# Kernel tuning notes

Measured on AMD Instinct MI355X. Metric: run time of the kernel, lower is better.

Reference implementation:

```python
import jax, jax.numpy as jnp
import numpy as np

EPS = 1e-5
GRID = 24          # GRID_SIZE
IMG = 96           # IMAGE_SIZE[0]
SCALE = IMG / GRID # 4.0
X0, X1 = -112.0, 224.0
Y0, Y1 = 0.0, 224.0
CIN = 48
CMID = 24
NKP = 4
B = 1024


def _conv(x, w):
    # x: [B,C,H,W], w: [O,I,kh,kw]
    return jax.lax.conv_general_dilated(x, w, (1, 1), 'SAME',
                                        dimension_numbers=('NCHW', 'OIHW', 'NCHW'))


def _head(x, w1, b1, g, be, m, v, w2, b2, sig):
    y = _conv(x, w1) + b1[None, :, None, None]
    inv = jax.lax.rsqrt(v + EPS)
    y = (y - m[None, :, None, None]) * (g * inv)[None, :, None, None] + be[None, :, None, None]
    y = jax.nn.relu(y)
    y = _conv(y, w2) + b2[None, :, None, None]
    return jax.nn.sigmoid(y) if sig else y


def _head_params(key, cout):
    ks = jax.random.split(key, 4)
    w1 = jax.random.normal(ks[0], (CMID, CIN, 3, 3), jnp.float32) * 0.05
    b1 = jnp.zeros((CMID,), jnp.float32)
    g = jnp.ones((CMID,), jnp.float32)
    be = jnp.zeros((CMID,), jnp.float32)
    m = jax.random.normal(ks[1], (CMID,), jnp.float32) * 0.1
    v = jax.random.uniform(ks[2], (CMID,), jnp.float32, 0.5, 1.5)
    w2 = jax.random.normal(ks[3], (cout, CMID, 1, 1), jnp.float32) * 0.05
    b2 = jnp.zeros((cout,), jnp.float32)
    return w1, b1, g, be, m, v, w2, b2


def setup_inputs() -> dict:
    key = jax.random.key(0)
    k0, kc, kk, kr, ko = jax.random.split(key, 5)
    d = {'features': jax.random.normal(k0, (B, CIN * GRID * GRID), jnp.float32)}
    for pref, kk_, cout in (('c', kc, 1), ('k', kk, NKP), ('r', kr, 2 * NKP), ('o', ko, 2 * NKP)):
        w1, b1, g, be, m, v, w2, b2 = _head_params(kk_, cout)
        d[pref + 'w1'], d[pref + 'b1'] = w1, b1
        d[pref + 'g'], d[pref + 'be'] = g, be
        d[pref + 'm'], d[pref + 'v'] = m, v
        d[pref + 'w2'], d[pref + 'b2'] = w2, b2
    return d


def reference(features,
              cw1, cb1, cg, cbe, cm, cv, cw2, cb2,
              kw1, kb1, kg, kbe, km, kv, kw2, kb2,
              rw1, rb1, rg, rbe, rm, rv, rw2, rb2,
              ow1, ob1, og, obe, om, ov, ow2, ob2):
    Bn = features.shape[0]
    x = features.reshape(Bn, CIN, GRID, GRID)
    center = _head(x, cw1, cb1, cg, cbe, cm, cv, cw2, cb2, True)    # [B,1,H,W]
    kp = _head(x, kw1, kb1, kg, kbe, km, kv, kw2, kb2, True)        # [B,N,H,W]
    reg = _head(x, rw1, rb1, rg, rbe, rm, rv, rw2, rb2, False)      # [B,2N,H,W]
    off = _head(x, ow1, ob1, og, obe, om, ov, ow2, ob2, False)      # [B,2N,H,W]

    H = W = GRID
    hm = kp.reshape(Bn, NKP, H * W)
    idx = jnp.argmax(hm, axis=2)                                   # [B,N]
    my = (idx // W).astype(jnp.float32)
    mx = (idx % W).astype(jnp.float32)
    # offset channels: (n*2) -> x, (n*2+1) -> y
    off_r = off.reshape(Bn, NKP, 2, H * W)
    g = jnp.take_along_axis(off_r, idx[:, :, None, None], axis=3)[..., 0]  # [B,N,2]
    ox, oy = g[..., 0], g[..., 1]
    fx = (mx + ox) * SCALE + X0
    fy = (my + oy) * SCALE + Y0
    pix = jnp.stack([fx, fy], axis=-1).reshape(Bn, 2 * NKP)        # [B,8]
    norm = jnp.stack([(fx - X0) / (X1 - X0), (fy - Y0) / (Y1 - Y0)], axis=-1).reshape(Bn, 2 * NKP)
    return (center, kp, reg, off, norm, pix)
```

## Files before the change

### kernel.cpp

```cpp
#include <hip/hip_runtime.h>
#include <stdint.h>

#define HW    576
#define CIN   48
#define NB    1024

#define O_CENTER 0L
#define O_KP     589824L
#define O_REG    2949120L
#define O_OFF    7667712L
#define O_NORM   12386304L
#define O_PIX    12394496L

#define WS_A1    0
#define WS_W2A   82944
#define WS_B1A   89088
#define WS_B2A   89472
#define WS_WKPT  89600
#define WS_B1KP  131072
#define WS_W2KP  131168
#define WS_B2KP  131552
#define WS_WOFFT 131584
#define WS_B1OFF 173056
#define WS_W2OFF 173152
#define WS_B2OFF 174688

typedef short bf16x8 __attribute__((ext_vector_type(8)));
typedef float f32x16 __attribute__((ext_vector_type(16)));

union U4B  { uint4 q; bf16x8 v; };
union U16Q { uint16_t u[8]; uint4 q; };
union U4Q  { uint16_t u[4]; uint2 q; };

__device__ __forceinline__ bf16x8 as_bf(uint4 q){ U4B u; u.q = q; return u.v; }
__device__ __forceinline__ uint16_t f2b(float f){
  union { float f; uint32_t i; } x; x.f = f;
  uint32_t r = x.i + 0x7FFFu + ((x.i >> 16) & 1u);
  return (uint16_t)(r >> 16);
}

struct P32 {
  const float* w1[4]; const float* b1[4]; const float* g[4]; const float* be[4];
  const float* m[4];  const float* v[4];  const float* w2[4]; const float* b2[4];
};

__device__ __forceinline__ void oc_decode(int oc, int& h, int& ch){
  if (oc == 0){ h = 0; ch = 0; }
  else if (oc < 5){ h = 1; ch = oc - 1; }
  else if (oc < 13){ h = 2; ch = oc - 5; }
  else { h = 3; ch = oc - 13; }
}

#define PREP_BLOCKS 48
__global__ void prep_kernel(P32 P, char* __restrict__ wsb){
  const int tid = threadIdx.x, bid = blockIdx.x;
  const int g0 = bid*256 + tid;
  const int STR = PREP_BLOCKS*256;
  __shared__ float sc[96], bfold[96];
  if (tid < 96){
    int h = tid / 24, o = tid % 24;
    float s = P.g[h][o] / sqrtf(P.v[h][o] + 1e-5f);
    sc[tid] = s;
    bfold[tid] = (P.b1[h][o] - P.m[h][o]) * s + P.be[h][o];
  }
  __syncthreads();
  uint16_t* A1 = (uint16_t*)(wsb + WS_A1);
  for (int t = g0; t < 41472; t += STR){
    int j = t & 7, slot = t >> 3;
    int row = slot % 96, sk = slot / 96;
    int g = sk & 1, k3 = (sk >> 1) % 3, sh = (sk >> 1) / 3;
    int ci = k3*16 + g*8 + j;
    int h = row / 24, o = row % 24;
    A1[t] = f2b(P.w1[h][(o*CIN + ci)*9 + sh] * sc[row]);
  }
  uint16_t* W2A = (uint16_t*)(wsb + WS_W2A);
  for (int t = g0; t < 3072; t += STR){
    int j = t & 7, slot = t >> 3;
    int oc = slot & 31, kg = slot >> 5;
    int k = kg*8 + j;
    float val = 0.f;
    if (oc < 21){
      int h, ch; oc_decode(oc, h, ch);
      int hk = k / 24, o = k % 24;
      if (hk == h) val = P.w2[h][ch*24 + o];
    }
    W2A[t] = f2b(val);
  }
  float* WKPT = (float*)(wsb + WS_WKPT);
  for (int t = g0; t < 10368; t += STR){
    int o = t % 24, k = (t/24) % 9, ci = t / 216;
    WKPT[t] = P.w1[1][(o*CIN + ci)*9 + k] * sc[24 + o];
  }
  float* WOFFT = (float*)(wsb + WS_WOFFT);
  for (int t = g0; t < 10368; t += STR){
    int o = t / 432;
    WOFFT[t] = P.w1[3][t] * sc[72 + o];
  }
  if (bid == 0){
    float* B1A = (float*)(wsb + WS_B1A);
    if (tid < 96) B1A[tid] = bfold[tid];
    float* B2A = (float*)(wsb + WS_B2A);
    if (tid < 32){
      float v = 0.f;
      if (tid < 21){ int h, ch; oc_decode(tid, h, ch); v = P.b2[h][ch]; }
      B2A[tid] = v;
    }
    if (tid < 24) ((float*)(wsb + WS_B1KP))[tid] = bfold[24 + tid];
    if (tid < 96) ((float*)(wsb + WS_W2KP))[tid] = P.w2[1][tid];
    if (tid < 4)  ((float*)(wsb + WS_B2KP))[tid] = P.b2[1][tid];
    if (tid < 24) ((float*)(wsb + WS_B1OFF))[tid] = bfold[72 + tid];
    for (int t = tid; t < 384; t += 256) ((float*)(wsb + WS_W2OFF))[t] = P.w2[3][t];
    if (tid < 16) ((float*)(wsb + WS_B2OFF))[tid] = P.b2[3][tid];
  }
}

__global__ __launch_bounds__(576) void conv_main(
    const float* __restrict__ feat, const char* __restrict__ wsb,
    float* __restrict__ out)
{
  __shared__ __align__(16) char smem[60000];
  const int b = blockIdx.x, tid = threadIdx.x;
  const int wave = tid >> 6, lane = tid & 63;
  const int q = lane >> 5, l31 = lane & 31;

  if (tid < 294){
    int cib = tid / 49, r = tid % 49;
    int slot = cib*625 + ((r < 25) ? r : (r - 24)*25);
    *(uint4*)(smem + slot*16) = make_uint4(0,0,0,0);
  }
  {
    const float* fb = feat + (size_t)b * (CIN*HW);
    int p = tid, py = p / 24, px = p % 24;
    int sbase = (py+1)*25 + (px+1);
    for (int cib = 0; cib < 6; ++cib){
      U16Q t8;
      #pragma unroll
      for (int j = 0; j < 8; ++j) t8.u[j] = f2b(fb[(cib*8 + j)*HW + p]);
      *(uint4*)(smem + (cib*625 + sbase)*16) = t8.q;
    }
  }
  __syncthreads();

  f32x16 acc[3][2] = {};
  const int p0 = wave*64 + l31, p1 = p0 + 32;
  const int py0 = p0/24, px0 = p0%24, py1 = p1/24, px1 = p1%24;
  const uint4* A1 = (const uint4*)(wsb + WS_A1);
  const uint4 zz = make_uint4(0,0,0,0);

  for (int sh = 0; sh < 9; ++sh){
    const int ky = sh / 3, kx = sh % 3;
    const int yb0 = py0 + ky, xb0 = px0 + kx;
    const int yb1 = py1 + ky, xb1 = px1 + kx;
    const bool v0 = (yb0 < 25) && (xb0 < 25);
    const bool v1 = (yb1 < 25) && (xb1 < 25);
    const int so0 = yb0*25 + xb0, so1 = yb1*25 + xb1;
    #pragma unroll
    for (int k3 = 0; k3 < 3; ++k3){
      const int cib = k3*2 + q;
      uint4 r0 = *(const uint4*)(smem + (cib*625 + (v0 ? so0 : 0))*16);
      uint4 r1 = *(const uint4*)(smem + (cib*625 + (v1 ? so1 : 0))*16);
      r0 = v0 ? r0 : zz;
      r1 = v1 ? r1 : zz;
      const bf16x8 bf0 = as_bf(r0), bf1 = as_bf(r1);
      const int abase = ((sh*3 + k3)*2 + q)*96 + l31;
      #pragma unroll
      for (int mt = 0; mt < 3; ++mt){
        const bf16x8 af = as_bf(A1[abase + mt*32]);
        acc[mt][0] = __builtin_amdgcn_mfma_f32_32x32x16_bf16(af, bf0, acc[mt][0], 0, 0, 0);
        acc[mt][1] = __builtin_amdgcn_mfma_f32_32x32x16_bf16(af, bf1, acc[mt][1], 0, 0, 0);
      }
    }
  }
  __syncthreads();

  const float* B1A = (const float*)(wsb + WS_B1A);
  const float* B2A = (const float*)(wsb + WS_B2A);
  const uint4* W2A = (const uint4*)(wsb + WS_W2A);
  char* ybuf = smem + wave*6144;

  #pragma unroll
  for (int st2 = 0; st2 < 2; ++st2){
    const int p = st2 ? p1 : p0;
    #pragma unroll
    for (int mt = 0; mt < 3; ++mt){
      #pragma unroll
      for (int rg = 0; rg < 4; ++rg){
        const int chanbase = mt*32 + rg*8 + q*4;
        const float* bp = B1A + chanbase;
        U4Q t4;
        #pragma unroll
        for (int r0 = 0; r0 < 4; ++r0){
          float y = acc[mt][st2][rg*4 + r0] + bp[r0];
          t4.u[r0] = f2b(fmaxf(y, 0.f));
        }
        *(uint2*)(ybuf + ((mt*4 + rg)*32 + l31)*16 + q*8) = t4.q;
      }
    }
    f32x16 c2 = {};
    #pragma unroll
    for (int k6 = 0; k6 < 6; ++k6){
      const bf16x8 yf = as_bf(*(const uint4*)(ybuf + ((k6*2 + q)*32 + l31)*16));
      const bf16x8 wf = as_bf(W2A[(k6*2 + q)*32 + l31]);
      c2 = __builtin_amdgcn_mfma_f32_32x32x16_bf16(wf, yf, c2, 0, 0, 0);
    }
    #pragma unroll
    for (int r = 0; r < 16; ++r){
      const int oc = (r & 3) + 8*(r >> 2) + 4*q;
      if (oc < 21){
        float v = c2[r] + B2A[oc];
        long base; int sig;
        if (oc == 0){ base = O_CENTER + (long)b*HW; sig = 1; }
        else if (oc < 5){ base = O_KP + ((long)b*4 + (oc-1))*HW; sig = 1; }
        else if (oc < 13){ base = O_REG + ((long)b*8 + (oc-5))*HW; sig = 0; }
        else { base = O_OFF + ((long)b*8 + (oc-13))*HW; sig = 0; }
        out[base + p] = sig ? (1.f / (1.f + __expf(-v))) : v;
      }
    }
  }
}

__global__ __launch_bounds__(576) void kp_select(
    const float* __restrict__ feat, const char* __restrict__ wsb,
    float* __restrict__ out)
{
  __shared__ __align__(16) float simg[8*26*24];
  __shared__ float wk_lds[8*9*24];
  __shared__ float ykp [96*24];
  __shared__ __align__(16) float opatch[4][432];
  __shared__ float ymidL[4*24];
  __shared__ int   jobL[4*HW];
  __shared__ int   KtotL;
  __shared__ unsigned long long bestL[4];

  const int b = blockIdx.x, tid = threadIdx.x;
  if (tid == 0) KtotL = 0;
  if (tid < 4) bestL[tid] = 0ULL;
  __syncthreads();

  if (tid < 256){
    const int n = tid >> 6, ln = tid & 63;
    const float* sp = out + O_KP + ((long)b*4 + n)*HW;
    float s[9];
    #pragma unroll
    for (int j = 0; j < 9; ++j) s[j] = sp[j*64 + ln];
    float mx = s[0];
    #pragma unroll
    for (int j = 1; j < 9; ++j) mx = fmaxf(mx, s[j]);
    #pragma unroll
    for (int off = 32; off >= 1; off >>= 1)
      mx = fmaxf(mx, __shfl_xor(mx, off, 64));
    const float sm = fminf(mx, 0.999999f);
    const float thr = sm / (sm + (1.f - sm) * 1.1331485f);
    #pragma unroll
    for (int j = 0; j < 9; ++j){
      if (s[j] >= thr){
        const int slot = atomicAdd(&KtotL, 1);
        jobL[slot] = (n << 16) | (j*64 + ln);
      }
    }
  }
  __syncthreads();
  const int Ktot = KtotL;

  const int s24 = tid / 24, omid = tid - s24*24;
  const int dst = (s24 + 1)*24 + omid;
  const float* fb = feat + (size_t)b * (CIN*HW);
  const float* WKPT = (const float*)(wsb + WS_WKPT);
  const float b1k = ((const float*)(wsb + WS_B1KP))[omid];

  for (int g0 = 0; g0 < Ktot; g0 += 96){
    const int Kg = min(96, Ktot - g0);

    int pyc[4], pxc[4];
    #pragma unroll
    for (int c = 0; c < 4; ++c){
      int p = 0;
      if (c*24 + s24 < Kg) p = jobL[g0 + c*24 + s24] & 0xFFFF;
      pyc[c] = p / 24; pxc[c] = p - (p/24)*24;
    }

    float acck[4] = {0.f,0.f,0.f,0.f};

    for (int pass = 0; pass < 6; ++pass){
      __syncthreads();
      if (tid < 384){
        int c = tid / 48, r = tid - c*48;
        int row = (r < 24) ? 0 : 25;
        int col = (r < 24) ? r : r - 24;
        simg[c*624 + row*24 + col] = 0.f;
      }
      #pragma unroll
      for (int c = 0; c < 8; ++c)
        simg[c*624 + dst] = fb[(pass*8 + c)*HW + tid];
      #pragma unroll
      for (int j = 0; j < 3; ++j)
        wk_lds[tid + j*576] = WKPT[pass*1728 + tid + j*576];
      __syncthreads();

      for (int c8 = 0; c8 < 8; ++c8){
        float pch[4][9];
        #pragma unroll
        for (int c = 0; c < 4; ++c) if (c*24 < Kg){
          const int a = c8*624 + pyc[c]*24 + pxc[c];
          const bool wl = (pxc[c] > 0), wr = (pxc[c] < 23);
          #pragma unroll
          for (int dr = 0; dr < 3; ++dr){
            const int aa = a + dr*24;
            pch[c][dr*3+0] = wl ? simg[aa-1] : 0.f;
            pch[c][dr*3+1] = simg[aa];
            pch[c][dr*3+2] = wr ? simg[aa+1] : 0.f;
          }
        }
        const float* wkb = wk_lds + c8*216 + omid;
        #pragma unroll
        for (int k = 0; k < 9; ++k){
          const float wk = wkb[k*24];
          #pragma unroll
          for (int c = 0; c < 4; ++c) if (c*24 < Kg)
            acck[c] = fmaf(pch[c][k], wk, acck[c]);
        }
      }
    }

    #pragma unroll
    for (int c = 0; c < 4; ++c) if (c*24 < Kg){
      const int sl = c*24 + s24;
      ykp[sl*24 + omid] = fmaxf(acck[c] + b1k, 0.f);
    }
    __syncthreads();

    if (tid < Kg){
      const int cand = g0 + tid;
      const int job = jobL[cand];
      const int n = job >> 16, p = job & 0xFFFF;
      const float* W2KP = (const float*)(wsb + WS_W2KP);
      float v = ((const float*)(wsb + WS_B2KP))[n];
      #pragma unroll
      for (int o = 0; o < 24; ++o)
        v = fmaf(ykp[tid*24 + o], W2KP[n*24 + o], v);
      union { float f; uint32_t u; } cv; cv.f = v;
      const uint32_t key = cv.u ^ (uint32_t)(((int32_t)cv.u >> 31) | (int32_t)0x80000000);
      const unsigned long long pk =
          ((unsigned long long)key << 32) | (unsigned)(1023 - p);
      atomicMax(&bestL[n], pk);
    }
    __syncthreads();
  }

  #pragma unroll
  for (int j = 0; j < 3; ++j){
    const int e = tid*3 + j;
    const int w = e / 432, idx = e - w*432;
    const int ci = idx / 9, k = idx - ci*9;
    const int p = 1023 - (int)(bestL[w] & 0xFFFFFFFFu);
    const int py = p / 24, px = p % 24;
    const int yy = py + k/3 - 1, xx = px + (k - (k/3)*3) - 1;
    float v = 0.f;
    if (yy >= 0 && yy < 24 && xx >= 0 && xx < 24)
      v = fb[ci*HW + yy*24 + xx];
    opatch[w][idx] = v;
  }
  __syncthreads();

  if (tid < 96){
    const int n = tid / 24, mid = tid - n*24;
    const float* wrow = (const float*)(wsb + WS_WOFFT) + mid*432;
    const float* prow = opatch[n];
    float s = 0.f;
    #pragma unroll 4
    for (int t = 0; t < 108; ++t){
      const float4 pv = *(const float4*)(prow + t*4);
      const float4 wv = *(const float4*)(wrow + t*4);
      s = fmaf(pv.x, wv.x, s);
      s = fmaf(pv.y, wv.y, s);
      s = fmaf(pv.z, wv.z, s);
      s = fmaf(pv.w, wv.w, s);
    }
    ymidL[n*24 + mid] = fmaxf(s + ((const float*)(wsb + WS_B1OFF))[mid], 0.f);
  }
  __syncthreads();

  if (tid < 4){
    const int n = tid;
    const int p = 1023 - (int)(bestL[n] & 0xFFFFFFFFu);
    const int py = p / 24, px = p % 24;
    const float* W2OFF = (const float*)(wsb + WS_W2OFF);
    const float* B2OFF = (const float*)(wsb + WS_B2OFF);
    float ox = B2OFF[2*n], oy = B2OFF[2*n + 1];
    #pragma unroll
    for (int o = 0; o < 24; ++o){
      const float ym = ymidL[n*24 + o];
      ox = fmaf(ym, W2OFF[(2*n)*24 + o], ox);
      oy = fmaf(ym, W2OFF[(2*n + 1)*24 + o], oy);
    }
    const float fx = ((float)px + ox) * 4.f - 112.f;
    const float fy = ((float)py + oy) * 4.f;
    out[O_NORM + b*8 + 2*n    ] = (fx + 112.f) * (1.f/336.f);
    out[O_NORM + b*8 + 2*n + 1] = fy * (1.f/224.f);
    out[O_PIX  + b*8 + 2*n    ] = fx;
    out[O_PIX  + b*8 + 2*n + 1] = fy;
  }
}

extern "C" void kernel_launch(void* const* d_in, const int* in_sizes, int n_in,
                              void* d_out, int out_size, void* d_ws, size_t ws_size,
                              hipStream_t stream)
{
  const float* feat = (const float*)d_in[0];
  P32 P;
  for (int h = 0; h < 4; ++h){
    const int base = 1 + h*8;
    P.w1[h] = (const float*)d_in[base+0];
    P.b1[h] = (const float*)d_in[base+1];
    P.g[h]  = (const float*)d_in[base+2];
    P.be[h] = (const float*)d_in[base+3];
    P.m[h]  = (const float*)d_in[base+4];
    P.v[h]  = (const float*)d_in[base+5];
    P.w2[h] = (const float*)d_in[base+6];
    P.b2[h] = (const float*)d_in[base+7];
  }
  char* wsb = (char*)d_ws;
  float* out = (float*)d_out;

  prep_kernel<<<dim3(PREP_BLOCKS), 256, 0, stream>>>(P, wsb);
  conv_main  <<<dim3(NB),          576, 0, stream>>>(feat, wsb, out);
  kp_select  <<<dim3(NB),          576, 0, stream>>>(feat, wsb, out);
}
```

Before: 569.5 us.

## Process pixel halves sequentially to cut accumulator registers and reuse ybuf per tile

```diff
diff --git a/kernel.cpp b/kernel.cpp
--- a/kernel.cpp
+++ b/kernel.cpp
@@ -118,7 +118,7 @@
     const float* __restrict__ feat, const char* __restrict__ wsb,
     float* __restrict__ out)
 {
-  __shared__ __align__(16) char smem[60000];
+  __shared__ __align__(16) char smem[78432];
   const int b = blockIdx.x, tid = threadIdx.x;
   const int wave = tid >> 6, lane = tid & 63;
   const int q = lane >> 5, l31 = lane & 31;
@@ -141,46 +141,41 @@
   }
   __syncthreads();
 
-  f32x16 acc[3][2] = {};
-  const int p0 = wave*64 + l31, p1 = p0 + 32;
-  const int py0 = p0/24, px0 = p0%24, py1 = p1/24, px1 = p1%24;
+  const int p0 = wave*64 + l31;
   const uint4* A1 = (const uint4*)(wsb + WS_A1);
-  const uint4 zz = make_uint4(0,0,0,0);
-
-  for (int sh = 0; sh < 9; ++sh){
-    const int ky = sh / 3, kx = sh % 3;
-    const int yb0 = py0 + ky, xb0 = px0 + kx;
-    const int yb1 = py1 + ky, xb1 = px1 + kx;
-    const bool v0 = (yb0 < 25) && (xb0 < 25);
-    const bool v1 = (yb1 < 25) && (xb1 < 25);
-    const int so0 = yb0*25 + xb0, so1 = yb1*25 + xb1;
-    #pragma unroll
-    for (int k3 = 0; k3 < 3; ++k3){
-      const int cib = k3*2 + q;
-      uint4 r0 = *(const uint4*)(smem + (cib*625 + (v0 ? so0 : 0))*16);
-      uint4 r1 = *(const uint4*)(smem + (cib*625 + (v1 ? so1 : 0))*16);
-      r0 = v0 ? r0 : zz;
-      r1 = v1 ? r1 : zz;
-      const bf16x8 bf0 = as_bf(r0), bf1 = as_bf(r1);
-      const int abase = ((sh*3 + k3)*2 + q)*96 + l31;
-      #pragma unroll
-      for (int mt = 0; mt < 3; ++mt){
-        const bf16x8 af = as_bf(A1[abase + mt*32]);
-        acc[mt][0] = __builtin_amdgcn_mfma_f32_32x32x16_bf16(af, bf0, acc[mt][0], 0, 0, 0);
-        acc[mt][1] = __builtin_amdgcn_mfma_f32_32x32x16_bf16(af, bf1, acc[mt][1], 0, 0, 0);
-      }
-    }
-  }
-  __syncthreads();
-
   const float* B1A = (const float*)(wsb + WS_B1A);
   const float* B2A = (const float*)(wsb + WS_B2A);
   const uint4* W2A = (const uint4*)(wsb + WS_W2A);
-  char* ybuf = smem + wave*6144;
-
-  #pragma unroll
+  char* ybuf = smem + 60000 + wave*2048;
+  const uint4 zz = make_uint4(0,0,0,0);
+
+  #pragma clang loop unroll(disable)
   for (int st2 = 0; st2 < 2; ++st2){
-    const int p = st2 ? p1 : p0;
+    const int p = p0 + st2*32;
+    const int py = p / 24, px = p % 24;
+    f32x16 acc[3] = {};
+
+    for (int sh = 0; sh < 9; ++sh){
+      const int ky = sh / 3, kx = sh % 3;
+      const int yb = py + ky, xb = px + kx;
+      const bool v = (yb < 25) && (xb < 25);
+      const int so = yb*25 + xb;
+      #pragma unroll
+      for (int k3 = 0; k3 < 3; ++k3){
+        const int cib = k3*2 + q;
+        uint4 r = *(const uint4*)(smem + (cib*625 + (v ? so : 0))*16);
+        r = v ? r : zz;
+        const bf16x8 bf = as_bf(r);
+        const int abase = ((sh*3 + k3)*2 + q)*96 + l31;
+        #pragma unroll
+        for (int mt = 0; mt < 3; ++mt){
+          const bf16x8 af = as_bf(A1[abase + mt*32]);
+          acc[mt] = __builtin_amdgcn_mfma_f32_32x32x16_bf16(af, bf, acc[mt], 0, 0, 0);
+        }
+      }
+    }
+
+    f32x16 c2 = {};
     #pragma unroll
     for (int mt = 0; mt < 3; ++mt){
       #pragma unroll
@@ -190,19 +185,20 @@
         U4Q t4;
         #pragma unroll
         for (int r0 = 0; r0 < 4; ++r0){
-          float y = acc[mt][st2][rg*4 + r0] + bp[r0];
+          float y = acc[mt][rg*4 + r0] + bp[r0];
           t4.u[r0] = f2b(fmaxf(y, 0.f));
         }
-        *(uint2*)(ybuf + ((mt*4 + rg)*32 + l31)*16 + q*8) = t4.q;
-      }
-    }
-    f32x16 c2 = {};
-    #pragma unroll
-    for (int k6 = 0; k6 < 6; ++k6){
-      const bf16x8 yf = as_bf(*(const uint4*)(ybuf + ((k6*2 + q)*32 + l31)*16));
-      const bf16x8 wf = as_bf(W2A[(k6*2 + q)*32 + l31]);
-      c2 = __builtin_amdgcn_mfma_f32_32x32x16_bf16(wf, yf, c2, 0, 0, 0);
-    }
+        *(uint2*)(ybuf + (rg*32 + l31)*16 + q*8) = t4.q;
+      }
+      #pragma unroll
+      for (int s = 0; s < 2; ++s){
+        const int k6 = mt*2 + s;
+        const bf16x8 yf = as_bf(*(const uint4*)(ybuf + ((s*2 + q)*32 + l31)*16));
+        const bf16x8 wf = as_bf(W2A[(k6*2 + q)*32 + l31]);
+        c2 = __builtin_amdgcn_mfma_f32_32x32x16_bf16(wf, yf, c2, 0, 0, 0);
+      }
+    }
+
     #pragma unroll
     for (int r = 0; r < 16; ++r){
       const int oc = (r & 3) + 8*(r >> 2) + 4*q;
```

Result: slower. 877.1 us (+54.0%).

## Gather per-candidate 3x3 patches instead of staging full image in kp_select

Applied to the files above, without the earlier changes.

```diff
diff --git a/kernel.cpp b/kernel.cpp
--- a/kernel.cpp
+++ b/kernel.cpp
@@ -88,8 +88,8 @@
   }
   float* WKPT = (float*)(wsb + WS_WKPT);
   for (int t = g0; t < 10368; t += STR){
-    int o = t % 24, k = (t/24) % 9, ci = t / 216;
-    WKPT[t] = P.w1[1][(o*CIN + ci)*9 + k] * sc[24 + o];
+    int o = t / 432;
+    WKPT[t] = P.w1[1][t] * sc[24 + o];
   }
   float* WOFFT = (float*)(wsb + WS_WOFFT);
   for (int t = g0; t < 10368; t += STR){
@@ -223,11 +223,8 @@
     const float* __restrict__ feat, const char* __restrict__ wsb,
     float* __restrict__ out)
 {
-  __shared__ __align__(16) float simg[8*26*24];
-  __shared__ float wk_lds[8*9*24];
-  __shared__ float ykp [96*24];
-  __shared__ __align__(16) float opatch[4][432];
-  __shared__ float ymidL[4*24];
+  __shared__ __align__(16) float patch[24*432];
+  __shared__ float ykp[24*24];
   __shared__ int   jobL[4*HW];
   __shared__ int   KtotL;
   __shared__ unsigned long long bestL[4];
@@ -262,79 +259,54 @@
   __syncthreads();
   const int Ktot = KtotL;
 
-  const int s24 = tid / 24, omid = tid - s24*24;
-  const int dst = (s24 + 1)*24 + omid;
   const float* fb = feat + (size_t)b * (CIN*HW);
   const float* WKPT = (const float*)(wsb + WS_WKPT);
-  const float b1k = ((const float*)(wsb + WS_B1KP))[omid];
-
-  for (int g0 = 0; g0 < Ktot; g0 += 96){
-    const int Kg = min(96, Ktot - g0);
-
-    int pyc[4], pxc[4];
-    #pragma unroll
-    for (int c = 0; c < 4; ++c){
-      int p = 0;
-      if (c*24 + s24 < Kg) p = jobL[g0 + c*24 + s24] & 0xFFFF;
-      pyc[c] = p / 24; pxc[c] = p - (p/24)*24;
-    }
-
-    float acck[4] = {0.f,0.f,0.f,0.f};
-
-    for (int pass = 0; pass < 6; ++pass){
-      __syncthreads();
-      if (tid < 384){
-        int c = tid / 48, r = tid - c*48;
-        int row = (r < 24) ? 0 : 25;
-        int col = (r < 24) ? r : r - 24;
-        simg[c*624 + row*24 + col] = 0.f;
-      }
-      #pragma unroll
-      for (int c = 0; c < 8; ++c)
-        simg[c*624 + dst] = fb[(pass*8 + c)*HW + tid];
-      #pragma unroll
-      for (int j = 0; j < 3; ++j)
-        wk_lds[tid + j*576] = WKPT[pass*1728 + tid + j*576];
-      __syncthreads();
-
-      for (int c8 = 0; c8 < 8; ++c8){
-        float pch[4][9];
-        #pragma unroll
-        for (int c = 0; c < 4; ++c) if (c*24 < Kg){
-          const int a = c8*624 + pyc[c]*24 + pxc[c];
-          const bool wl = (pxc[c] > 0), wr = (pxc[c] < 23);
-          #pragma unroll
-          for (int dr = 0; dr < 3; ++dr){
-            const int aa = a + dr*24;
-            pch[c][dr*3+0] = wl ? simg[aa-1] : 0.f;
-            pch[c][dr*3+1] = simg[aa];
-            pch[c][dr*3+2] = wr ? simg[aa+1] : 0.f;
-          }
-        }
-        const float* wkb = wk_lds + c8*216 + omid;
-        #pragma unroll
-        for (int k = 0; k < 9; ++k){
-          const float wk = wkb[k*24];
-          #pragma unroll
-          for (int c = 0; c < 4; ++c) if (c*24 < Kg)
-            acck[c] = fmaf(pch[c][k], wk, acck[c]);
-        }
-      }
-    }
-
-    #pragma unroll
-    for (int c = 0; c < 4; ++c) if (c*24 < Kg){
-      const int sl = c*24 + s24;
-      ykp[sl*24 + omid] = fmaxf(acck[c] + b1k, 0.f);
+  const float* B1KP = (const float*)(wsb + WS_B1KP);
+  const float* W2KP = (const float*)(wsb + WS_W2KP);
+  const float* B2KP = (const float*)(wsb + WS_B2KP);
+  const int ecand = tid / 24, emid = tid - ecand*24;
+
+  for (int g0 = 0; g0 < Ktot; g0 += 24){
+    const int Kg = min(24, Ktot - g0);
+
+    #pragma unroll
+    for (int j = 0; j < 18; ++j){
+      const int e = j*576 + tid;
+      const int cand = e / 432, idx = e - cand*432;
+      if (cand < Kg){
+        const int p = jobL[g0 + cand] & 0xFFFF;
+        const int py = p / 24, px = p % 24;
+        const int ci = idx / 9, k = idx - ci*9;
+        const int yy = py + k/3 - 1, xx = px + (k - (k/3)*3) - 1;
+        float v = 0.f;
+        if (yy >= 0 && yy < 24 && xx >= 0 && xx < 24)
+          v = fb[ci*HW + yy*24 + xx];
+        patch[cand*432 + idx] = v;
+      }
     }
     __syncthreads();
 
+    if (ecand < Kg){
+      const float* wrow = WKPT + emid*432;
+      const float* prow = patch + ecand*432;
+      float s = 0.f;
+      #pragma unroll 4
+      for (int t = 0; t < 108; ++t){
+        const float4 pv = *(const float4*)(prow + t*4);
+        const float4 wv = *(const float4*)(wrow + t*4);
+        s = fmaf(pv.x, wv.x, s);
+        s = fmaf(pv.y, wv.y, s);
+        s = fmaf(pv.z, wv.z, s);
+        s = fmaf(pv.w, wv.w, s);
+      }
+      ykp[ecand*24 + emid] = fmaxf(s + B1KP[emid], 0.f);
+    }
+    __syncthreads();
+
     if (tid < Kg){
-      const int cand = g0 + tid;
-      const int job = jobL[cand];
+      const int job = jobL[g0 + tid];
       const int n = job >> 16, p = job & 0xFFFF;
-      const float* W2KP = (const float*)(wsb + WS_W2KP);
-      float v = ((const float*)(wsb + WS_B2KP))[n];
+      float v = B2KP[n];
       #pragma unroll
       for (int o = 0; o < 24; ++o)
         v = fmaf(ykp[tid*24 + o], W2KP[n*24 + o], v);
@@ -347,6 +319,7 @@
     __syncthreads();
   }
 
+  float* opatch = patch;
   #pragma unroll
   for (int j = 0; j < 3; ++j){
     const int e = tid*3 + j;
@@ -358,14 +331,15 @@
     float v = 0.f;
     if (yy >= 0 && yy < 24 && xx >= 0 && xx < 24)
       v = fb[ci*HW + yy*24 + xx];
-    opatch[w][idx] = v;
-  }
-  __syncthreads();
-
+    opatch[w*432 + idx] = v;
+  }
+  __syncthreads();
+
+  float* ymidL = ykp;
   if (tid < 96){
     const int n = tid / 24, mid = tid - n*24;
     const float* wrow = (const float*)(wsb + WS_WOFFT) + mid*432;
-    const float* prow = opatch[n];
+    const float* prow = opatch + n*432;
     float s = 0.f;
     #pragma unroll 4
     for (int t = 0; t < 108; ++t){
```

Result: slower. 611.3 us (+7.3%).
